# Optimization experiments

Hardware: AMD Instinct MI355X
Metric: run time of the kernel (lower is better)

## Reference

```python
import jax, jax.numpy as jnp
import numpy as np

NEG_SLOPE = 0.2


def gat_conv(x, src, dst, W, asrc, adst, b):
    """Single-head PyG-style GATConv with self-loops.
    x: [N, din], src/dst: [E] int, W: [din, d], asrc/adst: [d], b: [d]."""
    N = x.shape[0]
    h = x @ W  # [N, d]
    alpha_s = h @ asrc  # [N]
    alpha_d = h @ adst  # [N]
    # add self loops so every node has at least one incoming edge
    loop = jnp.arange(N, dtype=src.dtype)
    srcf = jnp.concatenate([src, loop])
    dstf = jnp.concatenate([dst, loop])
    e = jax.nn.leaky_relu(alpha_s[srcf] + alpha_d[dstf], NEG_SLOPE)  # [E+N]
    m = jax.ops.segment_max(e, dstf, num_segments=N)
    ex = jnp.exp(e - m[dstf])
    denom = jax.ops.segment_sum(ex, dstf, num_segments=N)
    alpha = ex / denom[dstf]
    out = jax.ops.segment_sum(h[srcf] * alpha[:, None], dstf, num_segments=N)
    return out + b


def sdgnn_forward(x, edges, Wg, a_src, a_dst, bg, W1, b1, W2, b2):
    L = Wg.shape[0]
    R = Wg.shape[1]
    for l in range(L):
        feats = [x]
        for r in range(R):
            feats.append(gat_conv(x, edges[r, 0], edges[r, 1],
                                  Wg[l, r], a_src[l, r], a_dst[l, r], bg[l, r]))
        combined = jnp.concatenate(feats, axis=1)  # [N, 5*d]
        x = jnp.tanh(combined @ W1[l] + b1[l]) @ W2[l] + b2[l]
    return x


def setup_inputs() -> dict:
    key = jax.random.key(0)
    ks = jax.random.split(key, 8)
    N, D, E, L, R = 100000, 64, 1000000, 2, 4
    scale = 0.15  # ~kaiming for d=64
    x = jax.random.normal(ks[0], (N, D), dtype=jnp.float32)
    edges = jax.random.randint(ks[1], (R, 2, E), 0, N, dtype=jnp.int64)
    Wg = jax.random.normal(ks[2], (L, R, D, D), dtype=jnp.float32) * scale
    a_src = jax.random.normal(ks[3], (L, R, D), dtype=jnp.float32) * scale
    a_dst = jax.random.normal(ks[4], (L, R, D), dtype=jnp.float32) * scale
    bg = jnp.zeros((L, R, D), dtype=jnp.float32)
    W1 = jax.random.normal(ks[5], (L, 5 * D, D), dtype=jnp.float32) * 0.08
    b1 = jnp.zeros((L, D), dtype=jnp.float32)
    W2 = jax.random.normal(ks[6], (L, D, D), dtype=jnp.float32) * scale
    b2 = jnp.zeros((L, D), dtype=jnp.float32)
    return {"x": x, "edges": edges, "Wg": Wg, "a_src": a_src, "a_dst": a_dst,
            "bg": bg, "W1": W1, "b1": b1, "W2": W2, "b2": b2}


def reference(x, edges, Wg, a_src, a_dst, bg, W1, b1, W2, b2):
    return sdgnn_forward(x, edges, Wg, a_src, a_dst, bg, W1, b1, W2, b2)
```

## Files before the change

### kernel.cpp

```cpp
#include <hip/hip_runtime.h>
#include <hip/hip_bf16.h>
#include <math.h>

#define DD 64
#define RREL 4
#define LLAY 2
#define NEG_SLOPE 0.2f
#define EPB 4096
#define BSH 10
#define BSZ 1024

typedef __attribute__((ext_vector_type(8))) short short8;
typedef __attribute__((ext_vector_type(4))) short short4v;
typedef __attribute__((ext_vector_type(4))) float float4v;

__device__ __forceinline__ float lrelu(float x) { return x > 0.f ? x : NEG_SLOPE * x; }

__device__ __forceinline__ unsigned short f2bf(float f) {
    unsigned int u = __float_as_uint(f);
    return (unsigned short)((u + 0x7FFFu + ((u >> 16) & 1u)) >> 16);
}
__device__ __forceinline__ float bf2f(unsigned short u) {
    return __uint_as_float((unsigned int)u << 16);
}
__device__ __forceinline__ float bflo(unsigned int u) { return __uint_as_float(u << 16); }
__device__ __forceinline__ float bfhi(unsigned int u) {
    return __uint_as_float(u & 0xffff0000u);
}

__global__ void k_wvec(const float* __restrict__ Wg, const float* __restrict__ asrc,
                       const float* __restrict__ adst, float* __restrict__ wsrc,
                       float* __restrict__ wdst) {
    int idx = blockIdx.x * blockDim.x + threadIdx.x;
    if (idx >= LLAY * RREL * DD) return;
    int k = idx & 63;
    int lr = idx >> 6;
    const float* W = Wg + (size_t)lr * DD * DD;
    const float* as = asrc + lr * DD;
    const float* ad = adst + lr * DD;
    float s1 = 0.f, s2 = 0.f;
#pragma unroll
    for (int j = 0; j < DD; j++) {
        float w = W[k * DD + j];
        s1 += w * as[j];
        s2 += w * ad[j];
    }
    wsrc[idx] = s1;
    wdst[idx] = s2;
}

__global__ void k_prep(const float* __restrict__ Wg, const float* __restrict__ W1,
                       const float* __restrict__ W2, unsigned short* __restrict__ WgT,
                       unsigned short* __restrict__ W1T, unsigned short* __restrict__ W2T) {
    int idx = blockIdx.x * blockDim.x + threadIdx.x;
    if (idx < 8 * 4096) {
        int lr = idx >> 12, rem = idx & 4095, n = rem >> 6, k = rem & 63;
        WgT[idx] = f2bf(Wg[(size_t)lr * 4096 + k * 64 + n]);
    } else if (idx < 32768 + 2 * 64 * 320) {
        int i = idx - 32768;
        int l = i / 20480, rem = i % 20480, n = rem / 320, kk = rem % 320;
        int src;
        if (kk < 64) src = kk;
        else {
            int r = (kk - 64) >> 6, f = (kk - 64) & 63;
            src = 64 + r * 64 + ((f & 3) * 16) + (f >> 2);
        }
        W1T[i] = f2bf(W1[(size_t)l * 20480 + src * 64 + n]);
    } else if (idx < 32768 + 40960 + 2 * 4096) {
        int i = idx - 73728;
        int l = i >> 12, rem = i & 4095, n = rem >> 6, k = rem & 63;
        W2T[i] = f2bf(W2[(size_t)l * 4096 + k * 64 + n]);
    }
}

__global__ void k_copy_x(const float* __restrict__ x, unsigned short* __restrict__ combined,
                         int N) {
    int i = blockIdx.x * blockDim.x + threadIdx.x;
    if (i >= N * 32) return;
    int row = i >> 5, c2 = i & 31;
    float2 v = *(const float2*)(x + (size_t)row * DD + c2 * 2);
    unsigned int p = (unsigned int)f2bf(v.x) | ((unsigned int)f2bf(v.y) << 16);
    *(unsigned int*)(combined + (size_t)row * 320 + c2 * 2) = p;
}

__global__ void k_zero(int* __restrict__ p, int n) {
    int i = blockIdx.x * blockDim.x + threadIdx.x;
    if (i < n) p[i] = 0;
}

__global__ __launch_bounds__(256) void k_bhist(const int* __restrict__ edges,
                                               int* __restrict__ btot, int E, int NB) {
    int r = blockIdx.y;
    int e0 = blockIdx.x * EPB;
    int t = threadIdx.x;
    __shared__ int lh[128];
    for (int i = t; i < 128; i += 256) lh[i] = 0;
    __syncthreads();
    const int* dstp = edges + (size_t)r * 2 * E + E;
#pragma unroll
    for (int i = 0; i < EPB / 256; i++) {
        int e = e0 + t + 256 * i;
        if (e < E) atomicAdd(&lh[dstp[e] >> BSH], 1);
    }
    __syncthreads();
    for (int i = t; i < NB; i += 256) {
        int c = lh[i];
        if (c) atomicAdd(&btot[r * NB + i], c);
    }
}

__global__ void k_bscan(const int* __restrict__ btot, int* __restrict__ bucketoff,
                        int* __restrict__ bpos, int* __restrict__ csr_ptr, int N, int E, int NB) {
    int r = threadIdx.x;
    if (r >= RREL) return;
    int run = 0;
    for (int b = 0; b < NB; b++) {
        bucketoff[r * (NB + 1) + b] = run;
        bpos[r * NB + b] = run;
        run += btot[r * NB + b];
    }
    bucketoff[r * (NB + 1) + NB] = run;
    csr_ptr[(size_t)r * (N + 1) + N] = E;
}

__global__ __launch_bounds__(256) void k_binscatter(const int* __restrict__ edges,
                                                    int* __restrict__ bpos,
                                                    unsigned int* __restrict__ packed, int E,
                                                    int NB) {
    int r = blockIdx.y;
    int e0 = blockIdx.x * EPB;
    int t = threadIdx.x;
    __shared__ int lh[128], lbase[128];
    for (int i = t; i < 128; i += 256) lh[i] = 0;
    __syncthreads();
    const int* srcp = edges + (size_t)r * 2 * E;
    const int* dstp = srcp + E;
    int md[EPB / 256], ms[EPB / 256];
#pragma unroll
    for (int i = 0; i < EPB / 256; i++) {
        int e = e0 + t + 256 * i;
        int d = -1, s = 0;
        if (e < E) {
            d = dstp[e];
            s = srcp[e];
            atomicAdd(&lh[d >> BSH], 1);
        }
        md[i] = d;
        ms[i] = s;
    }
    __syncthreads();
    for (int i = t; i < NB; i += 256) {
        int c = lh[i];
        lbase[i] = c ? atomicAdd(&bpos[r * NB + i], c) : 0;
        lh[i] = 0;
    }
    __syncthreads();
#pragma unroll
    for (int i = 0; i < EPB / 256; i++) {
        if (md[i] >= 0) {
            int b = md[i] >> BSH;
            int p = lbase[b] + atomicAdd(&lh[b], 1);
            packed[(size_t)r * E + p] =
                ((unsigned int)(md[i] & (BSZ - 1)) << 17) | (unsigned int)ms[i];
        }
    }
}

__global__ __launch_bounds__(256) void k_bucket_sort(const unsigned int* __restrict__ packed,
                                                     const int* __restrict__ bucketoff,
                                                     int* __restrict__ csr_ptr,
                                                     int* __restrict__ csr_src, int N, int E,
                                                     int NB) {
    int r = blockIdx.y, b = blockIdx.x;
    int t = threadIdx.x;
    __shared__ int pos[BSZ];
    __shared__ int tsum[256];
    int base = bucketoff[r * (NB + 1) + b];
    int cnt = bucketoff[r * (NB + 1) + b + 1] - base;
    const unsigned int* pk = packed + (size_t)r * E + base;
    for (int i = t; i < BSZ; i += 256) pos[i] = 0;
    __syncthreads();
    for (int i = t; i < cnt; i += 256) atomicAdd(&pos[pk[i] >> 17], 1);
    __syncthreads();
    int v[4];
    int s = 0;
#pragma unroll
    for (int i = 0; i < 4; i++) {
        v[i] = pos[t * 4 + i];
        s += v[i];
    }
    tsum[t] = s;
    __syncthreads();
    for (int off = 1; off < 256; off <<= 1) {
        int add = (t >= off) ? tsum[t - off] : 0;
        __syncthreads();
        tsum[t] += add;
        __syncthreads();
    }
    int run = tsum[t] - s;
    __syncthreads();
#pragma unroll
    for (int i = 0; i < 4; i++) {
        int node_l = t * 4 + i;
        pos[node_l] = run;
        int node = b * BSZ + node_l;
        if (node < N) csr_ptr[(size_t)r * (N + 1) + node] = base + run;
        run += v[i];
    }
    __syncthreads();
    for (int i = t; i < cnt; i += 256) {
        unsigned int p = pk[i];
        int d = p >> 17;
        int sidx = p & 0x1FFFF;
        int loc = atomicAdd(&pos[d], 1);
        csr_src[(size_t)r * E + base + loc] = sidx;
    }
}


__global__ __launch_bounds__(256, 3) void k_hgemm(const unsigned short* __restrict__ X,
                                                  const unsigned short* __restrict__ WgTl,
                                                  const float* __restrict__ wsrcl,
                                                  const float* __restrict__ wdstl,
                                                  unsigned short* __restrict__ h4,
                                                  float* __restrict__ as4,
                                                  float* __restrict__ ad4, int N) {
    __shared__ __align__(16) unsigned short Xb[256][72];
    __shared__ __align__(16) unsigned short Wb[64][72];
    __shared__ float wsS[4][64], wdS[4][64];
    int tid = threadIdx.x, wave = tid >> 6, lane = tid & 63;
    int l15 = lane & 15, q = lane >> 4;
    int row0 = blockIdx.x * 256;
#pragma unroll
    for (int i = 0; i < 8; i++) {
        int f = tid + 256 * i;
        int rr = f >> 3, seg = f & 7;
        int grow = row0 + rr;
        short8 v = (short8){0, 0, 0, 0, 0, 0, 0, 0};
        if (grow < N) v = *(const short8*)(X + (size_t)grow * 320 + seg * 8);
        *(short8*)&Xb[rr][seg * 8] = v;
    }
    wsS[tid >> 6][tid & 63] = wsrcl[tid];
    wdS[tid >> 6][tid & 63] = wdstl[tid];
    __syncthreads();
    short8 afr[4][2];
#pragma unroll
    for (int mt = 0; mt < 4; mt++)
#pragma unroll
        for (int ks = 0; ks < 2; ks++)
            afr[mt][ks] = *(const short8*)&Xb[wave * 64 + mt * 16 + l15][ks * 32 + q * 8];
    {
        int grow = row0 + tid;
        float s[4] = {0.f, 0.f, 0.f, 0.f}, d[4] = {0.f, 0.f, 0.f, 0.f};
#pragma unroll
        for (int seg = 0; seg < 8; seg++) {
            short8 v = *(const short8*)&Xb[tid][seg * 8];
#pragma unroll
            for (int j = 0; j < 8; j++) {
                float xv = bf2f((unsigned short)v[j]);
                int k = seg * 8 + j;
#pragma unroll
                for (int r = 0; r < 4; r++) {
                    s[r] += xv * wsS[r][k];
                    d[r] += xv * wdS[r][k];
                }
            }
        }
        if (grow < N) {
#pragma unroll
            for (int r = 0; r < 4; r++) {
                as4[(size_t)r * N + grow] = s[r];
                ad4[(size_t)r * N + grow] = d[r];
            }
        }
    }
    for (int r = 0; r < 4; r++) {
        __syncthreads();
#pragma unroll
        for (int i = 0; i < 2; i++) {
            int f = tid + 256 * i;
            int n = f >> 3, seg = f & 7;
            *(short8*)&Wb[n][seg * 8] = *(const short8*)(WgTl + r * 4096 + n * 64 + seg * 8);
        }
        __syncthreads();
        short8 bfr[4][2];
#pragma unroll
        for (int nt = 0; nt < 4; nt++)
#pragma unroll
            for (int ks = 0; ks < 2; ks++)
                bfr[nt][ks] = *(const short8*)&Wb[nt * 16 + l15][ks * 32 + q * 8];
        float4v acc[4][4];
#pragma unroll
        for (int mt = 0; mt < 4; mt++)
#pragma unroll
            for (int nt = 0; nt < 4; nt++) acc[mt][nt] = (float4v){0.f, 0.f, 0.f, 0.f};
#pragma unroll
        for (int mt = 0; mt < 4; mt++)
#pragma unroll
            for (int nt = 0; nt < 4; nt++) {
                acc[mt][nt] = __builtin_amdgcn_mfma_f32_16x16x32_bf16(afr[mt][0], bfr[nt][0],
                                                                     acc[mt][nt], 0, 0, 0);
                acc[mt][nt] = __builtin_amdgcn_mfma_f32_16x16x32_bf16(afr[mt][1], bfr[nt][1],
                                                                     acc[mt][nt], 0, 0, 0);
            }
        unsigned short* hr = h4 + (size_t)r * N * 64;
#pragma unroll
        for (int mt = 0; mt < 4; mt++) {
            int rowb = row0 + wave * 64 + mt * 16 + q * 4;
#pragma unroll
            for (int reg = 0; reg < 4; reg++) {
                int row = rowb + reg;
                if (row < N) {
                    short4v sv;
                    sv[0] = (short)f2bf(acc[mt][0][reg]);
                    sv[1] = (short)f2bf(acc[mt][1][reg]);
                    sv[2] = (short)f2bf(acc[mt][2][reg]);
                    sv[3] = (short)f2bf(acc[mt][3][reg]);
                    *(short4v*)&hr[(size_t)row * 64 + l15 * 4] = sv;
                }
            }
        }
    }
}

template <bool BFOUT>
__global__ __launch_bounds__(256, 3) void k_mlp(const unsigned short* __restrict__ X,
                                                const unsigned short* __restrict__ W1Tl,
                                                const float* __restrict__ b1,
                                                const unsigned short* __restrict__ W2Tl,
                                                const float* __restrict__ b2,
                                                unsigned short* __restrict__ Ybf,
                                                float* __restrict__ Yf, int ldy, int N) {
    __shared__ __align__(16) unsigned short Xb[256][72];
    __shared__ __align__(16) unsigned short Wb[64][72];
    int tid = threadIdx.x, wave = tid >> 6, lane = tid & 63;
    int l15 = lane & 15, q = lane >> 4;
    int row0 = blockIdx.x * 256;
    float4v acc[4][4];
#pragma unroll
    for (int mt = 0; mt < 4; mt++)
#pragma unroll
        for (int nt = 0; nt < 4; nt++) acc[mt][nt] = (float4v){0.f, 0.f, 0.f, 0.f};
    for (int kc = 0; kc < 320; kc += 64) {
        __syncthreads();
#pragma unroll
        for (int i = 0; i < 8; i++) {
            int f = tid + 256 * i;
            int rr = f >> 3, seg = f & 7;
            int grow = row0 + rr;
            short8 v = (short8){0, 0, 0, 0, 0, 0, 0, 0};
            if (grow < N) v = *(const short8*)(X + (size_t)grow * 320 + kc + seg * 8);
            *(short8*)&Xb[rr][seg * 8] = v;
        }
#pragma unroll
        for (int i = 0; i < 2; i++) {
            int f = tid + 256 * i;
            int n = f >> 3, seg = f & 7;
            *(short8*)&Wb[n][seg * 8] = *(const short8*)(W1Tl + n * 320 + kc + seg * 8);
        }
        __syncthreads();
        short8 bfr[4][2];
#pragma unroll
        for (int nt = 0; nt < 4; nt++)
#pragma unroll
            for (int ks = 0; ks < 2; ks++)
                bfr[nt][ks] = *(const short8*)&Wb[nt * 16 + l15][ks * 32 + q * 8];
#pragma unroll
        for (int mt = 0; mt < 4; mt++) {
            short8 a0 = *(const short8*)&Xb[wave * 64 + mt * 16 + l15][q * 8];
            short8 a1 = *(const short8*)&Xb[wave * 64 + mt * 16 + l15][32 + q * 8];
#pragma unroll
            for (int nt = 0; nt < 4; nt++) {
                acc[mt][nt] =
                    __builtin_amdgcn_mfma_f32_16x16x32_bf16(a0, bfr[nt][0], acc[mt][nt], 0, 0, 0);
                acc[mt][nt] =
                    __builtin_amdgcn_mfma_f32_16x16x32_bf16(a1, bfr[nt][1], acc[mt][nt], 0, 0, 0);
            }
        }
    }
    __syncthreads();
#pragma unroll
    for (int mt = 0; mt < 4; mt++) {
        int rlb = wave * 64 + mt * 16 + q * 4;
#pragma unroll
        for (int reg = 0; reg < 4; reg++) {
#pragma unroll
            for (int nt = 0; nt < 4; nt++) {
                int n = nt * 16 + l15;
                Xb[rlb + reg][n] = f2bf(tanhf(acc[mt][nt][reg] + b1[n]));
            }
        }
    }
#pragma unroll
    for (int i = 0; i < 2; i++) {
        int f = tid + 256 * i;
        int n = f >> 3, seg = f & 7;
        *(short8*)&Wb[n][seg * 8] = *(const short8*)(W2Tl + n * 64 + seg * 8);
    }
    __syncthreads();
    short8 bfr[4][2];
#pragma unroll
    for (int nt = 0; nt < 4; nt++)
#pragma unroll
        for (int ks = 0; ks < 2; ks++)
            bfr[nt][ks] = *(const short8*)&Wb[nt * 16 + l15][ks * 32 + q * 8];
    float4v acc2[4][4];
#pragma unroll
    for (int mt = 0; mt < 4; mt++)
#pragma unroll
        for (int nt = 0; nt < 4; nt++) acc2[mt][nt] = (float4v){0.f, 0.f, 0.f, 0.f};
#pragma unroll
    for (int mt = 0; mt < 4; mt++) {
        short8 a0 = *(const short8*)&Xb[wave * 64 + mt * 16 + l15][q * 8];
        short8 a1 = *(const short8*)&Xb[wave * 64 + mt * 16 + l15][32 + q * 8];
#pragma unroll
        for (int nt = 0; nt < 4; nt++) {
            acc2[mt][nt] =
                __builtin_amdgcn_mfma_f32_16x16x32_bf16(a0, bfr[nt][0], acc2[mt][nt], 0, 0, 0);
            acc2[mt][nt] =
                __builtin_amdgcn_mfma_f32_16x16x32_bf16(a1, bfr[nt][1], acc2[mt][nt], 0, 0, 0);
        }
    }
#pragma unroll
    for (int mt = 0; mt < 4; mt++) {
        int rowb = row0 + wave * 64 + mt * 16 + q * 4;
#pragma unroll
        for (int reg = 0; reg < 4; reg++) {
            int row = rowb + reg;
            if (row < N) {
#pragma unroll
                for (int nt = 0; nt < 4; nt++) {
                    int n = nt * 16 + l15;
                    float v = acc2[mt][nt][reg] + b2[n];
                    if (BFOUT)
                        Ybf[(size_t)row * ldy + n] = f2bf(v);
                    else
                        Yf[(size_t)row * ldy + n] = v;
                }
            }
        }
    }
}

__device__ void gat_node_fullwave(int node, const int* __restrict__ csr_ptr,
                                  const int* __restrict__ csr_src,
                                  const unsigned short* __restrict__ h,
                                  const float* __restrict__ as_,
                                  const float* __restrict__ ad_, float bgv,
                                  unsigned short* __restrict__ out, int ldo, int lane) {
    float adv = ad_[node];
    float e_self = lrelu(as_[node] + adv);
    int beg = csr_ptr[node], end = csr_ptr[node + 1];
    int cnt = end - beg;

    if (cnt <= 64) {
        int s = 0;
        float e_lane = -3.0e38f;
        if (lane < cnt) {
            s = csr_src[beg + lane];
            e_lane = lrelu(as_[s] + adv);
        }
        float m = fmaxf(e_lane, e_self);
#pragma unroll
        for (int off = 32; off; off >>= 1) m = fmaxf(m, __shfl_xor(m, off));
        float p = (lane < cnt) ? expf(e_lane - m) : 0.f;
        float ssum = p;
#pragma unroll
        for (int off = 32; off; off >>= 1) ssum += __shfl_xor(ssum, off);
        float p_self = expf(e_self - m);
        float inv = 1.f / (ssum + p_self);
        float alpha = p * inv;
        float acc = p_self * inv * bf2f(h[(size_t)node * DD + lane]);
        for (int j0 = 0; j0 < cnt; ++j0) {
            int ss = __shfl(s, j0);
            float aa = __shfl(alpha, j0);
            acc += aa * bf2f(h[(size_t)ss * DD + lane]);
        }
        out[(size_t)node * ldo + lane] = f2bf(acc + bgv);
        return;
    }

    float m = e_self;
    for (int j = beg + lane; j < end; j += 64) m = fmaxf(m, lrelu(as_[csr_src[j]] + adv));
#pragma unroll
    for (int off = 32; off; off >>= 1) m = fmaxf(m, __shfl_xor(m, off));
    float ssum = 0.f;
    for (int j = beg + lane; j < end; j += 64) ssum += expf(lrelu(as_[csr_src[j]] + adv) - m);
#pragma unroll
    for (int off = 32; off; off >>= 1) ssum += __shfl_xor(ssum, off);
    ssum += expf(e_self - m);
    float inv = 1.f / ssum;
    float acc = expf(e_self - m) * inv * bf2f(h[(size_t)node * DD + lane]);
    for (int j0 = beg; j0 < end; j0 += 64) {
        int j = j0 + lane;
        int s = 0;
        float alpha = 0.f;
        if (j < end) {
            s = csr_src[j];
            alpha = expf(lrelu(as_[s] + adv) - m) * inv;
        }
        int c = end - j0;
        if (c > 64) c = 64;
        for (int t = 0; t < c; ++t) {
            int ss = __shfl(s, t);
            float aa = __shfl(alpha, t);
            acc += aa * bf2f(h[(size_t)ss * DD + lane]);
        }
    }
    out[(size_t)node * ldo + lane] = f2bf(acc + bgv);
}

__global__ __launch_bounds__(256) void k_gat(const int* __restrict__ csr_ptr4,
                                             const int* __restrict__ csr_src4,
                                             const unsigned short* __restrict__ h4,
                                             const float* __restrict__ as4,
                                             const float* __restrict__ ad4,
                                             const float* __restrict__ bg4,
                                             unsigned short* __restrict__ outbase, int ldo,
                                             int N, int E) {
    __shared__ int lsa_s[4][32][8];
    __shared__ float lsa_p[4][32][8];
    int lb = blockIdx.x;
    int r = (lb & 7) >> 1;
    int idx = ((lb >> 3) << 1) + (lb & 1);
    int wave = threadIdx.x >> 6, lane = threadIdx.x & 63;
    int oct = lane >> 3, lq = lane & 7;
    int nodeA = idx * 32 + wave * 8;
    if (nodeA >= N) return;
    int node = nodeA + oct;
    bool act = node < N;

    const int* csr_ptr = csr_ptr4 + (size_t)r * (N + 1);
    const int* csr_src = csr_src4 + (size_t)r * E;
    const unsigned short* h = h4 + (size_t)r * N * 64;
    const float* as_ = as4 + (size_t)r * N;
    const float* ad_ = ad4 + (size_t)r * N;
    const float* bg = bg4 + (size_t)r * DD;
    unsigned short* out = outbase + (size_t)64 * r;

    int beg = 0, cnt = 0;
    if (act) {
        beg = csr_ptr[node];
        cnt = csr_ptr[node + 1] - beg;
    }
    int m2 = max(cnt, __shfl_xor(cnt, 8));
    m2 = max(m2, __shfl_xor(m2, 16));
    int vmax = __builtin_amdgcn_readfirstlane(max(m2, __shfl_xor(m2, 32)));

    if (vmax <= 32) {
        bool in0 = lq < cnt, in1 = false, in2 = false, in3 = false;
        int s0 = in0 ? csr_src[beg + lq] : 0, s1 = 0, s2 = 0, s3 = 0;
        lsa_s[wave][lq][oct] = s0;
        if (vmax > 8) {
            in1 = (lq + 8) < cnt;
            s1 = in1 ? csr_src[beg + lq + 8] : 0;
            lsa_s[wave][lq + 8][oct] = s1;
        }
        if (vmax > 16) {
            in2 = (lq + 16) < cnt;
            s2 = in2 ? csr_src[beg + lq + 16] : 0;
            lsa_s[wave][lq + 16][oct] = s2;
        }
        if (vmax > 24) {
            in3 = (lq + 24) < cnt;
            s3 = in3 ? csr_src[beg + lq + 24] : 0;
            lsa_s[wave][lq + 24][oct] = s3;
        }
        float adv = act ? ad_[node] : 0.f;
        float e_self = act ? lrelu(as_[node] + adv) : 0.f;
        float p0 = in0 ? __expf(lrelu(as_[s0] + adv)) : 0.f;
        lsa_p[wave][lq][oct] = p0;
        float psum = p0;
        if (vmax > 8) {
            float p = in1 ? __expf(lrelu(as_[s1] + adv)) : 0.f;
            lsa_p[wave][lq + 8][oct] = p;
            psum += p;
        }
        if (vmax > 16) {
            float p = in2 ? __expf(lrelu(as_[s2] + adv)) : 0.f;
            lsa_p[wave][lq + 16][oct] = p;
            psum += p;
        }
        if (vmax > 24) {
            float p = in3 ? __expf(lrelu(as_[s3] + adv)) : 0.f;
            lsa_p[wave][lq + 24][oct] = p;
            psum += p;
        }
        float p_self = __expf(e_self);

        const char* hb = (const char*)h;
        unsigned lane16 = (unsigned)(lq << 4);
        uint4 hvs = make_uint4(0u, 0u, 0u, 0u);
        if (act) hvs = *(const uint4*)(hb + (((unsigned)node) << 7) + lane16);

        float a0 = 0.f, a1 = 0.f, a2 = 0.f, a3 = 0.f;
        float a4 = 0.f, a5 = 0.f, a6 = 0.f, a7 = 0.f;
        const int(*sp)[8] = &lsa_s[wave][0];
        const float(*pp)[8] = &lsa_p[wave][0];
        for (int j0 = 0; j0 < vmax; j0 += 8) {
#pragma unroll
            for (int g = 0; g < 2; g++) {
                if (j0 + g * 4 < vmax) {
#pragma unroll
                    for (int u = 0; u < 4; u++) {
                        int sv = sp[j0 + g * 4 + u][oct];
                        unsigned voff = ((unsigned)sv << 7) + lane16;
                        uint4 hv = *(const uint4*)(hb + voff);
                        float pw = pp[j0 + g * 4 + u][oct];
                        a0 += pw * bflo(hv.x);
                        a1 += pw * bfhi(hv.x);
                        a2 += pw * bflo(hv.y);
                        a3 += pw * bfhi(hv.y);
                        a4 += pw * bflo(hv.z);
                        a5 += pw * bfhi(hv.z);
                        a6 += pw * bflo(hv.w);
                        a7 += pw * bfhi(hv.w);
                    }
                }
            }
        }
        float ssum = psum;
#pragma unroll
        for (int off = 4; off; off >>= 1) ssum += __shfl_xor(ssum, off);
        float inv = __builtin_amdgcn_rcpf(ssum + p_self);

        if (act) {
            int b0 = 2 * lq;
            float o0 = (a0 + p_self * bflo(hvs.x)) * inv + bg[b0];
            float o1 = (a1 + p_self * bfhi(hvs.x)) * inv + bg[16 + b0];
            float o2 = (a2 + p_self * bflo(hvs.y)) * inv + bg[32 + b0];
            float o3 = (a3 + p_self * bfhi(hvs.y)) * inv + bg[48 + b0];
            float o4 = (a4 + p_self * bflo(hvs.z)) * inv + bg[b0 + 1];
            float o5 = (a5 + p_self * bfhi(hvs.z)) * inv + bg[16 + b0 + 1];
            float o6 = (a6 + p_self * bflo(hvs.w)) * inv + bg[32 + b0 + 1];
            float o7 = (a7 + p_self * bfhi(hvs.w)) * inv + bg[48 + b0 + 1];
            uint4 pck;
            pck.x = (unsigned int)f2bf(o0) | ((unsigned int)f2bf(o1) << 16);
            pck.y = (unsigned int)f2bf(o2) | ((unsigned int)f2bf(o3) << 16);
            pck.z = (unsigned int)f2bf(o4) | ((unsigned int)f2bf(o5) << 16);
            pck.w = (unsigned int)f2bf(o6) | ((unsigned int)f2bf(o7) << 16);
            *(uint4*)(out + (size_t)node * ldo + 8 * lq) = pck;
        }
        return;
    }

    float bgv = bg[((lane & 3) << 4) | (lane >> 2)];
#pragma unroll
    for (int k = 0; k < 8; k++) {
        if (nodeA + k < N)
            gat_node_fullwave(nodeA + k, csr_ptr, csr_src, h, as_, ad_, bgv, out, ldo, lane);
    }
}

extern "C" void kernel_launch(void* const* d_in, const int* in_sizes, int n_in,
                              void* d_out, int out_size, void* d_ws, size_t ws_size,
                              hipStream_t stream) {
    const float* x = (const float*)d_in[0];
    const int* edges = (const int*)d_in[1];
    const float* Wg = (const float*)d_in[2];
    const float* a_src = (const float*)d_in[3];
    const float* a_dst = (const float*)d_in[4];
    const float* bg = (const float*)d_in[5];
    const float* W1 = (const float*)d_in[6];
    const float* b1 = (const float*)d_in[7];
    const float* W2 = (const float*)d_in[8];
    const float* b2 = (const float*)d_in[9];
    float* out = (float*)d_out;

    const int N = in_sizes[0] / DD;
    const int E = in_sizes[1] / (2 * RREL);
    const int NB = (N + BSZ - 1) >> BSH;

    size_t off = 0;
    auto alloc = [&](size_t bytes) {
        size_t o = off;
        off = (off + bytes + 255) & ~(size_t)255;
        return o;
    };
    char* ws = (char*)d_ws;
    unsigned short* combined = (unsigned short*)(ws + alloc((size_t)N * 320 * 2));
    unsigned short* h4 = (unsigned short*)(ws + alloc((size_t)4 * N * 64 * 2));
    float* wsrc = (float*)(ws + alloc(LLAY * RREL * DD * 4));
    float* wdst = (float*)(ws + alloc(LLAY * RREL * DD * 4));
    unsigned short* WgT = (unsigned short*)(ws + alloc(8 * 4096 * 2));
    unsigned short* W1T = (unsigned short*)(ws + alloc(2 * 64 * 320 * 2));
    unsigned short* W2T = (unsigned short*)(ws + alloc(2 * 4096 * 2));
    int* btot = (int*)(ws + alloc((size_t)RREL * NB * 4));
    int* bucketoff = (int*)(ws + alloc((size_t)RREL * (NB + 1) * 4));
    int* bpos = (int*)(ws + alloc((size_t)RREL * NB * 4));
    unsigned int* packed = (unsigned int*)(ws + alloc((size_t)RREL * E * 4));
    int* csr_ptr = (int*)(ws + alloc((size_t)RREL * (N + 1) * 4));
    int* csr_src = (int*)(ws + alloc((size_t)RREL * E * 4));
    (void)ws_size;
    float* as4 = (float*)packed;
    float* ad4 = as4 + (size_t)4 * N;

    const int ebblocks = (E + EPB - 1) / EPB;

    k_zero<<<dim3((RREL * NB + 255) / 256), dim3(256), 0, stream>>>(btot, RREL * NB);
    k_wvec<<<dim3(2), dim3(256), 0, stream>>>(Wg, a_src, a_dst, wsrc, wdst);
    k_prep<<<dim3(320), dim3(256), 0, stream>>>(Wg, W1, W2, WgT, W1T, W2T);
    k_copy_x<<<dim3((N * 32 + 255) / 256), dim3(256), 0, stream>>>(x, combined, N);
    k_bhist<<<dim3(ebblocks, RREL), dim3(256), 0, stream>>>(edges, btot, E, NB);
    k_bscan<<<dim3(1), dim3(64), 0, stream>>>(btot, bucketoff, bpos, csr_ptr, N, E, NB);
    k_binscatter<<<dim3(ebblocks, RREL), dim3(256), 0, stream>>>(edges, bpos, packed, E, NB);
    k_bucket_sort<<<dim3(NB, RREL), dim3(256), 0, stream>>>(packed, bucketoff, csr_ptr, csr_src,
                                                            N, E, NB);

    const int gemm_blocks = (N + 255) / 256;
    const int bpr = (N + 31) / 32;
    const int gat_grid = 8 * ((bpr + 1) / 2);

    for (int l = 0; l < LLAY; l++) {
        k_hgemm<<<dim3(gemm_blocks), dim3(256), 0, stream>>>(
            combined, WgT + (size_t)l * 4 * 4096, wsrc + l * 256, wdst + l * 256, h4, as4, ad4, N);
        k_gat<<<dim3(gat_grid), dim3(256), 0, stream>>>(
            csr_ptr, csr_src, h4, as4, ad4, bg + (size_t)l * RREL * DD,
            combined + 64, 320, N, E);
        if (l == LLAY - 1) {
            k_mlp<false><<<dim3(gemm_blocks), dim3(256), 0, stream>>>(
                combined, W1T + (size_t)l * 20480, b1 + l * DD, W2T + (size_t)l * 4096,
                b2 + l * DD, nullptr, out, DD, N);
        } else {
            k_mlp<true><<<dim3(gemm_blocks), dim3(256), 0, stream>>>(
                combined, W1T + (size_t)l * 20480, b1 + l * DD, W2T + (size_t)l * 4096,
                b2 + l * DD, combined, nullptr, 320, N);
        }
    }
}
```

Measured before the change: 454.6 us.

## Sort GAT nodes by in-degree so waves process uniform-degree nodes

Adds a counting sort of nodes by in-degree (histogram, scan and scatter kernels) that builds a per-relation permutation. The GAT kernel then walks nodes in permuted order, so the 8 nodes sharing a wave have similar edge counts. This is meant to cut divergence and wasted lanes in the small-degree path and keep high-degree nodes together. In exchange it adds three small preprocessing kernels, an extra indirection per node, and scattered output writes and h/csr_ptr access from the permuted order.

```diff
diff --git a/kernel.cpp b/kernel.cpp
--- a/kernel.cpp
+++ b/kernel.cpp
@@ -9,6 +9,7 @@
 #define EPB 4096
 #define BSH 10
 #define BSZ 1024
+#define DBINS 34
 
 typedef __attribute__((ext_vector_type(8))) short short8;
 typedef __attribute__((ext_vector_type(4))) short short4v;
@@ -110,7 +111,9 @@
 }
 
 __global__ void k_bscan(const int* __restrict__ btot, int* __restrict__ bucketoff,
-                        int* __restrict__ bpos, int* __restrict__ csr_ptr, int N, int E, int NB) {
+                        int* __restrict__ bpos, int* __restrict__ csr_ptr,
+                        int* __restrict__ dbins, int N, int E, int NB) {
+    for (int i = threadIdx.x; i < RREL * DBINS; i += 64) dbins[i] = 0;
     int r = threadIdx.x;
     if (r >= RREL) return;
     int run = 0;
@@ -214,6 +217,78 @@
         int sidx = p & 0x1FFFF;
         int loc = atomicAdd(&pos[d], 1);
         csr_src[(size_t)r * E + base + loc] = sidx;
+    }
+}
+
+__global__ __launch_bounds__(256) void k_dhist(const int* __restrict__ csr_ptr4,
+                                               int* __restrict__ dbins, int N) {
+    int r = blockIdx.y;
+    __shared__ int lh[DBINS];
+    int t = threadIdx.x;
+    if (t < DBINS) lh[t] = 0;
+    __syncthreads();
+    const int* cp = csr_ptr4 + (size_t)r * (N + 1);
+    int n0 = blockIdx.x * 4096;
+#pragma unroll
+    for (int i = 0; i < 16; i++) {
+        int n = n0 + t + 256 * i;
+        if (n < N) {
+            int deg = cp[n + 1] - cp[n];
+            atomicAdd(&lh[deg <= 32 ? deg : 33], 1);
+        }
+    }
+    __syncthreads();
+    if (t < DBINS) {
+        int c = lh[t];
+        if (c) atomicAdd(&dbins[r * DBINS + t], c);
+    }
+}
+
+__global__ void k_dscan(const int* __restrict__ dbins, int* __restrict__ dpos) {
+    int r = threadIdx.x;
+    if (r >= RREL) return;
+    int run = 0;
+    for (int b = 0; b < DBINS; b++) {
+        dpos[r * DBINS + b] = run;
+        run += dbins[r * DBINS + b];
+    }
+}
+
+__global__ __launch_bounds__(256) void k_dscatter(const int* __restrict__ csr_ptr4,
+                                                  int* __restrict__ dpos,
+                                                  int* __restrict__ perm, int N) {
+    int r = blockIdx.y;
+    __shared__ int lh[DBINS], lbase[DBINS];
+    int t = threadIdx.x;
+    if (t < DBINS) lh[t] = 0;
+    __syncthreads();
+    const int* cp = csr_ptr4 + (size_t)r * (N + 1);
+    int n0 = blockIdx.x * 4096;
+    int bins[16];
+#pragma unroll
+    for (int i = 0; i < 16; i++) {
+        int n = n0 + t + 256 * i;
+        int b = -1;
+        if (n < N) {
+            int deg = cp[n + 1] - cp[n];
+            b = deg <= 32 ? deg : 33;
+            atomicAdd(&lh[b], 1);
+        }
+        bins[i] = b;
+    }
+    __syncthreads();
+    if (t < DBINS) {
+        int c = lh[t];
+        lbase[t] = c ? atomicAdd(&dpos[r * DBINS + t], c) : 0;
+        lh[t] = 0;
+    }
+    __syncthreads();
+#pragma unroll
+    for (int i = 0; i < 16; i++) {
+        if (bins[i] >= 0) {
+            int loc = lbase[bins[i]] + atomicAdd(&lh[bins[i]], 1);
+            perm[(size_t)r * N + loc] = n0 + t + 256 * i;
+        }
     }
 }
 
@@ -512,6 +587,7 @@
 
 __global__ __launch_bounds__(256) void k_gat(const int* __restrict__ csr_ptr4,
                                              const int* __restrict__ csr_src4,
+                                             const int* __restrict__ perm4,
                                              const unsigned short* __restrict__ h4,
                                              const float* __restrict__ as4,
                                              const float* __restrict__ ad4,
@@ -527,17 +603,19 @@
     int oct = lane >> 3, lq = lane & 7;
     int nodeA = idx * 32 + wave * 8;
     if (nodeA >= N) return;
-    int node = nodeA + oct;
-    bool act = node < N;
+    int pos = nodeA + oct;
+    bool act = pos < N;
 
     const int* csr_ptr = csr_ptr4 + (size_t)r * (N + 1);
     const int* csr_src = csr_src4 + (size_t)r * E;
+    const int* perm = perm4 + (size_t)r * N;
     const unsigned short* h = h4 + (size_t)r * N * 64;
     const float* as_ = as4 + (size_t)r * N;
     const float* ad_ = ad4 + (size_t)r * N;
     const float* bg = bg4 + (size_t)r * DD;
     unsigned short* out = outbase + (size_t)64 * r;
 
+    int node = act ? perm[pos] : 0;
     int beg = 0, cnt = 0;
     if (act) {
         beg = csr_ptr[node];
@@ -647,8 +725,10 @@
     float bgv = bg[((lane & 3) << 4) | (lane >> 2)];
 #pragma unroll
     for (int k = 0; k < 8; k++) {
-        if (nodeA + k < N)
-            gat_node_fullwave(nodeA + k, csr_ptr, csr_src, h, as_, ad_, bgv, out, ldo, lane);
+        if (nodeA + k < N) {
+            int nk = perm[nodeA + k];
+            gat_node_fullwave(nk, csr_ptr, csr_src, h, as_, ad_, bgv, out, ldo, lane);
+        }
     }
 }
 
@@ -691,21 +771,28 @@
     unsigned int* packed = (unsigned int*)(ws + alloc((size_t)RREL * E * 4));
     int* csr_ptr = (int*)(ws + alloc((size_t)RREL * (N + 1) * 4));
     int* csr_src = (int*)(ws + alloc((size_t)RREL * E * 4));
+    int* perm = (int*)(ws + alloc((size_t)RREL * N * 4));
+    int* dbins = (int*)(ws + alloc((size_t)RREL * DBINS * 4));
+    int* dpos = (int*)(ws + alloc((size_t)RREL * DBINS * 4));
     (void)ws_size;
     float* as4 = (float*)packed;
     float* ad4 = as4 + (size_t)4 * N;
 
     const int ebblocks = (E + EPB - 1) / EPB;
+    const int nblocks4k = (N + 4095) / 4096;
 
     k_zero<<<dim3((RREL * NB + 255) / 256), dim3(256), 0, stream>>>(btot, RREL * NB);
     k_wvec<<<dim3(2), dim3(256), 0, stream>>>(Wg, a_src, a_dst, wsrc, wdst);
     k_prep<<<dim3(320), dim3(256), 0, stream>>>(Wg, W1, W2, WgT, W1T, W2T);
     k_copy_x<<<dim3((N * 32 + 255) / 256), dim3(256), 0, stream>>>(x, combined, N);
     k_bhist<<<dim3(ebblocks, RREL), dim3(256), 0, stream>>>(edges, btot, E, NB);
-    k_bscan<<<dim3(1), dim3(64), 0, stream>>>(btot, bucketoff, bpos, csr_ptr, N, E, NB);
+    k_bscan<<<dim3(1), dim3(64), 0, stream>>>(btot, bucketoff, bpos, csr_ptr, dbins, N, E, NB);
     k_binscatter<<<dim3(ebblocks, RREL), dim3(256), 0, stream>>>(edges, bpos, packed, E, NB);
     k_bucket_sort<<<dim3(NB, RREL), dim3(256), 0, stream>>>(packed, bucketoff, csr_ptr, csr_src,
                                                             N, E, NB);
+    k_dhist<<<dim3(nblocks4k, RREL), dim3(256), 0, stream>>>(csr_ptr, dbins, N);
+    k_dscan<<<dim3(1), dim3(64), 0, stream>>>(dbins, dpos);
+    k_dscatter<<<dim3(nblocks4k, RREL), dim3(256), 0, stream>>>(csr_ptr, dpos, perm, N);
 
     const int gemm_blocks = (N + 255) / 256;
     const int bpr = (N + 31) / 32;
@@ -715,7 +802,7 @@
         k_hgemm<<<dim3(gemm_blocks), dim3(256), 0, stream>>>(
             combined, WgT + (size_t)l * 4 * 4096, wsrc + l * 256, wdst + l * 256, h4, as4, ad4, N);
         k_gat<<<dim3(gat_grid), dim3(256), 0, stream>>>(
-            csr_ptr, csr_src, h4, as4, ad4, bg + (size_t)l * RREL * DD,
+            csr_ptr, csr_src, perm, h4, as4, ad4, bg + (size_t)l * RREL * DD,
             combined + 64, 320, N, E);
         if (l == LLAY - 1) {
             k_mlp<false><<<dim3(gemm_blocks), dim3(256), 0, stream>>>(
```

New measurement: 485.2 us. 1.07x slower.
